# Kernel tuning notes

Hardware: AMD Instinct MI355X
Metric: run time of the kernel (lower is better)

## Reference

```python
import jax, jax.numpy as jnp
import numpy as np

B, L, D = 4, 2048, 512
NL, ED, N, R, K = 2, 1024, 16, 32, 4
EPS = 1e-5


def rmsnorm(x, w):
    return x * jax.lax.rsqrt(jnp.mean(x * x, axis=-1, keepdims=True) + EPS) * w


def mamba_block(u, in_w, conv_w, conv_b, xproj_w, dtproj_w, dtproj_b, A_log, Dp, out_w):
    # u: [B, L, D]
    xz = u @ in_w.T                              # [B, L, 2*ED]
    xp, z = jnp.split(xz, 2, axis=-1)
    # depthwise causal conv1d over time
    xc = jnp.transpose(xp, (0, 2, 1))            # [B, ED, L]
    w = conv_w[:, None, :]                       # [ED, 1, K]
    xc = jax.lax.conv_general_dilated(
        xc, w, window_strides=(1,), padding=[(K - 1, 0)],
        feature_group_count=ED, dimension_numbers=('NCH', 'OIH', 'NCH'))
    xc = jnp.transpose(xc, (0, 2, 1)) + conv_b   # [B, L, ED]
    xc = jax.nn.silu(xc)
    # input-dependent SSM params
    dbc = xc @ xproj_w.T                         # [B, L, R+2N]
    dt, Bm, Cm = jnp.split(dbc, [R, R + N], axis=-1)
    delta = jax.nn.softplus(dt @ dtproj_w.T + dtproj_b)  # [B, L, ED]
    A = -jnp.exp(A_log)                          # [ED, N]
    # sequential selective scan over time (carry h: [B, ED, N])
    dT = jnp.transpose(delta, (1, 0, 2))
    BT = jnp.transpose(Bm, (1, 0, 2))
    CT = jnp.transpose(Cm, (1, 0, 2))
    xT = jnp.transpose(xc, (1, 0, 2))

    def step(h, inp):
        d_t, B_t, C_t, x_t = inp                 # [B,ED], [B,N], [B,N], [B,ED]
        dA = jnp.exp(d_t[..., None] * A)         # [B, ED, N]
        h = dA * h + (d_t * x_t)[..., None] * B_t[:, None, :]
        y = jnp.einsum('ben,bn->be', h, C_t)
        return h, y

    h0 = jnp.zeros((u.shape[0], ED, N), u.dtype)
    _, yT = jax.lax.scan(step, h0, (dT, BT, CT, xT))
    y = jnp.transpose(yT, (1, 0, 2)) + Dp * xc   # [B, L, ED]
    y = y * jax.nn.silu(z)
    return y @ out_w.T                           # [B, L, D]


def setup_inputs() -> dict:
    key = jax.random.key(0)
    ks = jax.random.split(key, 10)
    s = 0.02
    return {
        'x': jax.random.normal(ks[0], (B, L, D), jnp.float32),
        'mask': jnp.ones((B, L), jnp.int32),
        'norm_w': jnp.ones((NL, D), jnp.float32),
        'in_w': jax.random.normal(ks[1], (NL, 2 * ED, D), jnp.float32) * s,
        'conv_w': jax.random.normal(ks[2], (NL, ED, K), jnp.float32) * 0.2,
        'conv_b': jnp.zeros((NL, ED), jnp.float32),
        'xproj_w': jax.random.normal(ks[3], (NL, R + 2 * N, ED), jnp.float32) * s,
        'dtproj_w': jax.random.normal(ks[4], (NL, ED, R), jnp.float32) * s,
        'dtproj_b': jax.random.normal(ks[5], (NL, ED), jnp.float32) * 0.1,
        'A_log': jnp.broadcast_to(jnp.log(jnp.arange(1, N + 1, dtype=jnp.float32)), (NL, ED, N)) + 0.0,
        'D_param': jnp.ones((NL, ED), jnp.float32),
        'out_w': jax.random.normal(ks[6], (NL, D, ED), jnp.float32) * s,
    }


def reference(x, mask, norm_w, in_w, conv_w, conv_b, xproj_w, dtproj_w,
              dtproj_b, A_log, D_param, out_w):
    m = mask.astype(x.dtype)[:, :, None]
    for i in range(norm_w.shape[0]):
        x = x * m
        # ResidualBlock: x + MambaBlock(RMSNorm(x)); dropout is identity at eval
        x = x + mamba_block(rmsnorm(x, norm_w[i]), in_w[i], conv_w[i], conv_b[i],
                            xproj_w[i], dtproj_w[i], dtproj_b[i], A_log[i],
                            D_param[i], out_w[i])
        x = x * m
    return x, x[:, 0, :]
```

## Files before the change

kernel.cpp:

```cpp
#include <hip/hip_runtime.h>
#include <math.h>

#define B_ 4
#define L_ 2048
#define D_ 512
#define ED_ 1024
#define N_ 16
#define R_ 32
#define KC_ 4
#define M_ (B_*L_)
#define NC_ 128
#define T_  (L_/NC_)
#define S_  (B_*ED_*N_)
#define LOG2E 1.44269504f
#define LN2   0.69314718f

typedef __attribute__((ext_vector_type(8))) short short8;
typedef __attribute__((ext_vector_type(4))) float floatx4;
typedef __attribute__((ext_vector_type(2))) float floatv2;

static __device__ __forceinline__ float b2f(unsigned short u) {
    unsigned int v = ((unsigned int)u) << 16;
    float f;
    __builtin_memcpy(&f, &v, 4);
    return f;
}
static __device__ __forceinline__ unsigned short f2b(float f) {
    unsigned int u;
    __builtin_memcpy(&u, &f, 4);
    unsigned int lsb = (u >> 16) & 1u;
    u += 0x7fffu + lsb;
    return (unsigned short)(u >> 16);
}
static __device__ __forceinline__ float silu(float x) {
    return x / (1.f + exp2f(-LOG2E * x));
}
static __device__ __forceinline__ float softplusf(float x) {
    return fmaxf(x, 0.f) + LN2 * log2f(1.f + exp2f(-LOG2E * fabsf(x)));
}
static __device__ __forceinline__ void pow_tree2(float a1, floatv2* pw) {
    float a2 = a1 * a1, a4 = a2 * a2, a8 = a4 * a4;
    pw[0] = (floatv2){a1, a2};
    pw[1] = pw[0] * a2;
    pw[2] = pw[0] * a4;
    pw[3] = pw[1] * a4;
    pw[4] = pw[0] * a8;
    pw[5] = pw[1] * a8;
    pw[6] = pw[2] * a8;
    pw[7] = pw[3] * a8;
}

__global__ void k_flag0(int* flag) {
    if (blockIdx.x == 0 && threadIdx.x == 0) *flag = 0;
}
__global__ void k_detect(const unsigned short* __restrict__ x, int* flag) {
    int i = blockIdx.x * 256 + threadIdx.x;
    unsigned int e = (x[i] >> 7) & 0xFF;
    unsigned long long m = __ballot(e >= 0x88);
    if ((threadIdx.x & 63) == 0 && m != 0ull) atomicOr(flag, 1);
}

struct Seg9 { const void* src[9]; int prefix[10]; };
__global__ void k_cvt_batch(Seg9 segs, float* __restrict__ dst, int total,
                            const int* __restrict__ flag) {
    int i = blockIdx.x * 256 + threadIdx.x;
    if (i >= total) return;
    int s = 0;
#pragma unroll
    for (int k = 1; k < 9; ++k) if (i >= segs.prefix[k]) s = k;
    int off = i - segs.prefix[s];
    if (*flag) dst[i] = ((const float*)segs.src[s])[off];
    else       dst[i] = b2f(((const unsigned short*)segs.src[s])[off]);
}
__global__ void k_cvt_bf_batch(const void* __restrict__ src0,
                               const void* __restrict__ src1,
                               unsigned short* __restrict__ dst,
                               int n0, int total, const int* __restrict__ flag) {
    int i = blockIdx.x * 256 + threadIdx.x;
    if (i >= total) return;
    const void* src = (i < n0) ? src0 : src1;
    int off = (i < n0) ? i : i - n0;
    if (*flag) dst[i] = f2b(((const float*)src)[off]);
    else       dst[i] = ((const unsigned short*)src)[off];
}

__global__ void k_prep(const float* __restrict__ wdt,
                       const float* __restrict__ A_log,
                       float* __restrict__ wT,
                       float* __restrict__ A0s,
                       int* __restrict__ structf) {
    int idx = blockIdx.x * 256 + threadIdx.x;
    int layer = idx >> 10, e = idx & (ED_ - 1);
    const float* src = wdt + (size_t)idx * R_;
    float* dstb = wT + (size_t)layer * (R_ * ED_);
#pragma unroll
    for (int r = 0; r < R_; ++r)
        dstb[(r >> 2) * (ED_ * 4) + e * 4 + (r & 3)] = src[r];
    float A0 = -exp2f(LOG2E * A_log[(size_t)idx * N_]) * LOG2E;
    bool st = true;
#pragma unroll
    for (int n = 1; n < N_; ++n) {
        float An = -exp2f(LOG2E * A_log[(size_t)idx * N_ + n]) * LOG2E;
        st = st && (fabsf(An - (n + 1) * A0) <= 1e-4f * fabsf(An));
    }
    A0s[idx] = A0;
    structf[idx] = st ? 1 : 0;
}

__global__ __launch_bounds__(128) void k_rmsnorm(float* __restrict__ x,
                                                 const int* __restrict__ mask,
                                                 const float* __restrict__ w,
                                                 unsigned short* __restrict__ ubf) {
    int row = blockIdx.x;
    int tid = threadIdx.x;
    size_t base = (size_t)row * D_ + tid * 4;
    float4 v = *(const float4*)(x + base);
    float mv = (float)mask[row];
    v.x *= mv; v.y *= mv; v.z *= mv; v.w *= mv;
    *(float4*)(x + base) = v;
    float ss = v.x*v.x + v.y*v.y + v.z*v.z + v.w*v.w;
#pragma unroll
    for (int o = 1; o < 64; o <<= 1) ss += __shfl_xor(ss, o, 64);
    __shared__ float sred[2];
    if ((tid & 63) == 0) sred[tid >> 6] = ss;
    __syncthreads();
    float rs = rsqrtf((sred[0] + sred[1]) / (float)D_ + 1e-5f);
    float4 wv = *(const float4*)(w + tid * 4);
    ushort4 b4;
    b4.x = f2b(v.x * rs * wv.x);
    b4.y = f2b(v.y * rs * wv.y);
    b4.z = f2b(v.z * rs * wv.z);
    b4.w = f2b(v.w * rs * wv.w);
    *(ushort4*)(ubf + base) = b4;
}

typedef __attribute__((address_space(1))) const unsigned int guint;
typedef __attribute__((address_space(3))) unsigned int luint;
#define GLL(gp, lp) __builtin_amdgcn_global_load_lds((guint*)(const void*)(gp), (luint*)(void*)(lp), 16, 0, 0)

template<int N> static __device__ __forceinline__ void waitv() {
    if constexpr (N == 0) asm volatile("s_waitcnt vmcnt(0)" ::: "memory");
    else if constexpr (N == 3) asm volatile("s_waitcnt vmcnt(3)" ::: "memory");
    else if constexpr (N == 4) asm volatile("s_waitcnt vmcnt(4)" ::: "memory");
}

template<int MODE, int BNT>
__global__ __launch_bounds__(256) void gemm_bt(const unsigned short* __restrict__ A,
                                               const unsigned short* __restrict__ W,
                                               void* __restrict__ C,
                                               const int* __restrict__ mask,
                                               const int* __restrict__ flag,
                                               void* __restrict__ out,
                                               int M, int N, int K) {
    constexpr int NF = BNT / 32;
    constexpr int LW = 2 + BNT / 64;
    __shared__ unsigned short As[3][128][32];
    __shared__ unsigned short Bs[3][BNT][32];
    int tid  = threadIdx.x;
    int wave = tid >> 6;
    int lane = tid & 63;
    int nwg = gridDim.x * gridDim.y;
    int id  = blockIdx.y * gridDim.x + blockIdx.x;
    int swz = (id & 7) * (nwg >> 3) + (id >> 3);
    int m0 = (swz / gridDim.x) * 128;
    int n0 = (swz % gridDim.x) * BNT;
    int wm = (wave & 1) * 64;
    int wn = (wave >> 1) * (BNT / 2);
    int quad = lane >> 4;
    int l16  = lane & 15;
    int crd = (quad ^ ((l16 >> 1) & 3)) * 8;

    int rA0 = wave * 16 + (lane >> 2);
    int cA  = ((lane & 3) ^ ((rA0 >> 1) & 3)) * 8;

    floatx4 acc[4][NF] = {};

    auto stage = [&](int buf, int k0) {
        const unsigned short* gA0 = A + (size_t)(m0 + rA0) * K + k0 + cA;
        GLL(gA0,                   &As[buf][wave * 16][0]);
        GLL(gA0 + (size_t)64 * K,  &As[buf][64 + wave * 16][0]);
        const unsigned short* gB0 = W + (size_t)(n0 + rA0) * K + k0 + cA;
        GLL(gB0,                   &Bs[buf][wave * 16][0]);
        if constexpr (BNT == 128)
            GLL(gB0 + (size_t)64 * K, &Bs[buf][64 + wave * 16][0]);
    };

    int nk = K / 32;
    stage(0, 0);
    stage(1, 32);

    int cur = 0;
    for (int t = 0; t < nk; ++t) {
        if (t + 1 < nk) waitv<LW>();
        else            waitv<0>();
        asm volatile("s_barrier" ::: "memory");
        if (t + 2 < nk) {
            int bw = cur + 2; if (bw >= 3) bw -= 3;
            stage(bw, (t + 2) * 32);
        }
        short8 af[4], bfr[NF];
#pragma unroll
        for (int f = 0; f < 4; ++f)
            af[f]  = *(const short8*)&As[cur][wm + f * 16 + l16][crd];
#pragma unroll
        for (int f = 0; f < NF; ++f)
            bfr[f] = *(const short8*)&Bs[cur][wn + f * 16 + l16][crd];
#pragma unroll
        for (int mf = 0; mf < 4; ++mf)
#pragma unroll
            for (int nf = 0; nf < NF; ++nf)
                acc[mf][nf] = __builtin_amdgcn_mfma_f32_16x16x32_bf16(af[mf], bfr[nf], acc[mf][nf], 0, 0, 0);
        asm volatile("s_waitcnt lgkmcnt(0)" ::: "memory");
        cur = (cur == 2) ? 0 : cur + 1;
    }

    int fl = (MODE == 3) ? *flag : 0;
#pragma unroll
    for (int mf = 0; mf < 4; ++mf) {
#pragma unroll
        for (int nf = 0; nf < NF; ++nf) {
#pragma unroll
            for (int i = 0; i < 4; ++i) {
                int r = m0 + wm + mf * 16 + quad * 4 + i;
                int c = n0 + wn + nf * 16 + l16;
                size_t idx = (size_t)r * N + c;
                if (MODE == 1) {
                    ((unsigned short*)C)[idx] = f2b(acc[mf][nf][i]);
                } else if (MODE == 2) {
                    float* C32 = (float*)C;
                    float mv = (float)mask[r];
                    C32[idx] = (C32[idx] + acc[mf][nf][i]) * mv;
                } else {
                    const float* C32 = (const float*)C;
                    float mv = (float)mask[r];
                    float v = (C32[idx] + acc[mf][nf][i]) * mv;
                    if (fl) ((float*)out)[idx] = v;
                    else    ((unsigned short*)out)[idx] = f2b(v);
                    if ((r & (L_ - 1)) == 0) {
                        size_t oidx = (size_t)M_ * D_ + (size_t)(r >> 11) * D_ + c;
                        if (fl) ((float*)out)[oidx] = v;
                        else    ((unsigned short*)out)[oidx] = f2b(v);
                    }
                }
            }
        }
    }
}

#define BM 64
#define BN 64
#define BK 16
#define KS 8
__global__ __launch_bounds__(256) void gemm_nt_sk(const float* __restrict__ A,
                                                  const float* __restrict__ W,
                                                  float* __restrict__ part,
                                                  int M, int N, int K) {
    __shared__ float Asm[BK][BM + 4];
    __shared__ float Wsm[BK][BN + 4];
    int tid = threadIdx.x;
    int ks = blockIdx.x;
    int m0 = blockIdx.y * BM;
    int kb = ks * (K / KS);
    int ke = kb + (K / KS);
    int tx = tid & 15;
    int ty = tid >> 4;
    int lr = tid >> 2;
    int lk = (tid & 3) * 4;
    float acc[4][4] = {};
    for (int k0 = kb; k0 < ke; k0 += BK) {
        float4 av = *(const float4*)(A + (size_t)(m0 + lr) * K + k0 + lk);
        Asm[lk + 0][lr] = av.x; Asm[lk + 1][lr] = av.y;
        Asm[lk + 2][lr] = av.z; Asm[lk + 3][lr] = av.w;
        float4 wv = *(const float4*)(W + (size_t)lr * K + k0 + lk);
        Wsm[lk + 0][lr] = wv.x; Wsm[lk + 1][lr] = wv.y;
        Wsm[lk + 2][lr] = wv.z; Wsm[lk + 3][lr] = wv.w;
        __syncthreads();
#pragma unroll
        for (int kk = 0; kk < BK; ++kk) {
            float4 a = *(const float4*)&Asm[kk][ty * 4];
            float4 w = *(const float4*)&Wsm[kk][tx * 4];
            acc[0][0] += a.x * w.x; acc[0][1] += a.x * w.y; acc[0][2] += a.x * w.z; acc[0][3] += a.x * w.w;
            acc[1][0] += a.y * w.x; acc[1][1] += a.y * w.y; acc[1][2] += a.y * w.z; acc[1][3] += a.y * w.w;
            acc[2][0] += a.z * w.x; acc[2][1] += a.z * w.y; acc[2][2] += a.z * w.z; acc[2][3] += a.z * w.w;
            acc[3][0] += a.w * w.x; acc[3][1] += a.w * w.y; acc[3][2] += a.w * w.z; acc[3][3] += a.w * w.w;
        }
        __syncthreads();
    }
    float* p = part + (size_t)ks * M * N;
#pragma unroll
    for (int i = 0; i < 4; ++i) {
        int m = m0 + ty * 4 + i;
#pragma unroll
        for (int j = 0; j < 4; ++j) {
            int n = tx * 4 + j;
            p[(size_t)m * N + n] = acc[i][j];
        }
    }
}

__global__ void k_red8(const float* __restrict__ part, float* __restrict__ dbc, int mn4) {
    int i = blockIdx.x * 256 + threadIdx.x;
    if (i >= mn4) return;
    float4 s = ((const float4*)part)[i];
#pragma unroll
    for (int ks = 1; ks < KS; ++ks) {
        float4 v = ((const float4*)(part + (size_t)ks * mn4 * 4))[i];
        s.x += v.x; s.y += v.y; s.z += v.z; s.w += v.w;
    }
    ((float4*)dbc)[i] = s;
}

__global__ __launch_bounds__(256) void k_conv(const unsigned short* __restrict__ xzb,
                                              const float* __restrict__ cw,
                                              const float* __restrict__ cb,
                                              float* __restrict__ xc) {
    int idx = blockIdx.x * 256 + threadIdx.x;
    int e2 = idx & (ED_ / 2 - 1);
    int e  = e2 * 2;
    int bl = idx >> 9;
    int l  = bl & (L_ - 1);
    float acc0 = cb[e], acc1 = cb[e + 1];
    const unsigned short* col = xzb + (size_t)bl * (2 * ED_) + e;
    float4 wa = *(const float4*)(cw + e * 4);
    float4 wb = *(const float4*)(cw + e * 4 + 4);
    ushort2 v3 = *(const ushort2*)(col);
    if (l >= 3) {
        ushort2 v0 = *(const ushort2*)(col - 3 * 2 * ED_);
        ushort2 v1 = *(const ushort2*)(col - 2 * 2 * ED_);
        ushort2 v2 = *(const ushort2*)(col - 1 * 2 * ED_);
        acc0 += wa.x * b2f(v0.x) + wa.y * b2f(v1.x) + wa.z * b2f(v2.x) + wa.w * b2f(v3.x);
        acc1 += wb.x * b2f(v0.y) + wb.y * b2f(v1.y) + wb.z * b2f(v2.y) + wb.w * b2f(v3.y);
    } else {
        if (l >= 2) {
            ushort2 v1 = *(const ushort2*)(col - 2 * 2 * ED_);
            acc0 += wa.y * b2f(v1.x); acc1 += wb.y * b2f(v1.y);
        }
        if (l >= 1) {
            ushort2 v2 = *(const ushort2*)(col - 1 * 2 * ED_);
            acc0 += wa.z * b2f(v2.x); acc1 += wb.z * b2f(v2.y);
        }
        acc0 += wa.w * b2f(v3.x); acc1 += wb.w * b2f(v3.y);
    }
    float2 o; o.x = silu(acc0); o.y = silu(acc1);
    *(float2*)(xc + (size_t)bl * ED_ + e) = o;
}

__global__ __launch_bounds__(256) void k_scan_a(const float* __restrict__ xc,
                                                const float* __restrict__ dbc,
                                                const float* __restrict__ wt,
                                                const float* __restrict__ dtb,
                                                const float* __restrict__ A0s,
                                                const int* __restrict__ structf,
                                                const float* __restrict__ A_log,
                                                float* __restrict__ sumdbuf,
                                                float* __restrict__ hl) {
    int b = blockIdx.z, c = blockIdx.y;
    int e = blockIdx.x * 256 + threadIdx.x;
    __shared__ float sRow[T_][64];
    size_t t0 = (size_t)b * L_ + (size_t)c * T_;
    {
        const float4* src = (const float4*)(dbc + t0 * 64);
        ((float4*)&sRow[0][0])[threadIdx.x] = src[threadIdx.x];
    }
    __syncthreads();
    floatv2 w2[R_ / 2];
    {
        const float4* wtp = (const float4*)wt;
#pragma unroll
        for (int i = 0; i < 8; ++i) {
            float4 v = wtp[(size_t)i * ED_ + e];
            w2[2 * i]     = (floatv2){v.x, v.y};
            w2[2 * i + 1] = (floatv2){v.z, v.w};
        }
    }
    float bias = dtb[e];
    float A0 = A0s[e];
    bool structured = structf[e] != 0;
    floatv2 h2[8];
#pragma unroll
    for (int i = 0; i < 8; ++i) h2[i] = (floatv2){0.f, 0.f};
    float sumd = 0.f;
    if (structured) {
        const float* xp = xc + t0 * ED_ + e;
        float xv_t = *xp; xp += ED_;
        for (int t = 0; t < T_; ++t) {
            float xv_n = (t + 1 < T_) ? *xp : 0.f; xp += ED_;
            const floatv2* dt2 = (const floatv2*)&sRow[t][0];
            floatv2 q0 = {0.f, 0.f}, q1 = {0.f, 0.f}, q2 = {0.f, 0.f}, q3 = {0.f, 0.f};
#pragma unroll
            for (int r = 0; r < R_ / 2; r += 4) {
                q0 += dt2[r + 0] * w2[r + 0];
                q1 += dt2[r + 1] * w2[r + 1];
                q2 += dt2[r + 2] * w2[r + 2];
                q3 += dt2[r + 3] * w2[r + 3];
            }
            floatv2 qs = (q0 + q1) + (q2 + q3);
            float d = softplusf(qs.x + qs.y + bias);
            float dx = d * xv_t;
            sumd += d;
            floatv2 pw[8];
            pow_tree2(exp2f(d * A0), pw);
            const floatv2* bb2 = (const floatv2*)&sRow[t][32];
#pragma unroll
            for (int i = 0; i < 8; ++i)
                h2[i] = pw[i] * h2[i] + dx * bb2[i];
            xv_t = xv_n;
        }
    } else {
        float A[N_];
        float* h = (float*)h2;
#pragma unroll
        for (int n = 0; n < N_; ++n) A[n] = -exp2f(LOG2E * A_log[e * N_ + n]) * LOG2E;
        float* wsc = (float*)w2;
        for (int t = 0; t < T_; ++t) {
            size_t bl = t0 + t;
            float p0 = bias, p1 = 0.f, p2 = 0.f, p3 = 0.f;
#pragma unroll
            for (int r = 0; r < R_; r += 4) {
                p0 += sRow[t][r + 0] * wsc[r + 0];
                p1 += sRow[t][r + 1] * wsc[r + 1];
                p2 += sRow[t][r + 2] * wsc[r + 2];
                p3 += sRow[t][r + 3] * wsc[r + 3];
            }
            float d = softplusf((p0 + p1) + (p2 + p3));
            float dx = d * xc[bl * ED_ + e];
            sumd += d;
#pragma unroll
            for (int n = 0; n < N_; ++n) {
                float a = exp2f(d * A[n]);
                h[n] = a * h[n] + dx * sRow[t][32 + n];
            }
        }
    }
    size_t s = (size_t)c * S_ + ((size_t)b * ED_ + e) * N_;
    const float* h = (const float*)h2;
#pragma unroll
    for (int n = 0; n < N_; ++n) hl[s + n] = h[n];
    sumdbuf[(size_t)c * (B_ * ED_) + (size_t)b * ED_ + e] = sumd;
}

__global__ __launch_bounds__(256) void k_scan_b(const float* __restrict__ sumd,
                                                const float* __restrict__ hl,
                                                const float* __restrict__ A_log,
                                                float* __restrict__ carry) {
    int s = blockIdx.x * 256 + threadIdx.x;
    float An = -exp2f(LOG2E * A_log[s & (ED_ * N_ - 1)]) * LOG2E;
    int be = s >> 4;
    float sdr[8], hlr[8];
#pragma unroll
    for (int c = 0; c < 8; ++c) {
        sdr[c] = sumd[(size_t)c * (B_ * ED_) + be];
        hlr[c] = hl[(size_t)c * S_ + s];
    }
    float h = 0.f;
#pragma unroll
    for (int c = 0; c < NC_; ++c) {
        int r = c & 7;
        carry[(size_t)c * S_ + s] = h;
        float p = exp2f(sdr[r] * An), q = hlr[r];
        if (c + 8 < NC_) {
            sdr[r] = sumd[(size_t)(c + 8) * (B_ * ED_) + be];
            hlr[r] = hl[(size_t)(c + 8) * S_ + s];
        }
        h = p * h + q;
    }
}

__global__ __launch_bounds__(256) void k_scan_c(const float* __restrict__ xc,
                                                const float* __restrict__ dbc,
                                                const unsigned short* __restrict__ xzb,
                                                const float* __restrict__ wt,
                                                const float* __restrict__ dtb,
                                                const float* __restrict__ A0s,
                                                const int* __restrict__ structf,
                                                const float* __restrict__ A_log,
                                                const float* __restrict__ Dp,
                                                const float* __restrict__ carry,
                                                unsigned short* __restrict__ ybf) {
    int b = blockIdx.z, c = blockIdx.y;
    int e = blockIdx.x * 256 + threadIdx.x;
    __shared__ float sRow[T_][64];
    size_t t0 = (size_t)b * L_ + (size_t)c * T_;
    {
        const float4* src = (const float4*)(dbc + t0 * 64);
        ((float4*)&sRow[0][0])[threadIdx.x] = src[threadIdx.x];
    }
    __syncthreads();
    floatv2 w2[R_ / 2];
    {
        const float4* wtp = (const float4*)wt;
#pragma unroll
        for (int i = 0; i < 8; ++i) {
            float4 v = wtp[(size_t)i * ED_ + e];
            w2[2 * i]     = (floatv2){v.x, v.y};
            w2[2 * i + 1] = (floatv2){v.z, v.w};
        }
    }
    float bias = dtb[e];
    float A0 = A0s[e];
    bool structured = structf[e] != 0;
    floatv2 h2[8];
    size_t s = (size_t)c * S_ + ((size_t)b * ED_ + e) * N_;
    {
        const floatv2* cp = (const floatv2*)(carry + s);
#pragma unroll
        for (int i = 0; i < 8; ++i) h2[i] = cp[i];
    }
    float Dv = Dp[e];
    if (structured) {
        const float* xp  = xc  + t0 * ED_ + e;
        const unsigned short* zp = xzb + t0 * (2 * ED_) + ED_ + e;
        unsigned short* yp = ybf + t0 * ED_ + e;
        float xv_t = *xp;  xp  += ED_;
        unsigned short z_t = *zp; zp += 2 * ED_;
        for (int t = 0; t < T_; ++t) {
            float xv_n = 0.f;
            unsigned short z_n = 0;
            if (t + 1 < T_) {
                xv_n = *xp;
                z_n  = *zp;
            }
            xp += ED_; zp += 2 * ED_;
            const floatv2* dt2 = (const floatv2*)&sRow[t][0];
            floatv2 q0 = {0.f, 0.f}, q1 = {0.f, 0.f}, q2 = {0.f, 0.f}, q3 = {0.f, 0.f};
#pragma unroll
            for (int r = 0; r < R_ / 2; r += 4) {
                q0 += dt2[r + 0] * w2[r + 0];
                q1 += dt2[r + 1] * w2[r + 1];
                q2 += dt2[r + 2] * w2[r + 2];
                q3 += dt2[r + 3] * w2[r + 3];
            }
            floatv2 qs = (q0 + q1) + (q2 + q3);
            float d_t = softplusf(qs.x + qs.y + bias);
            float dx = d_t * xv_t;
            floatv2 pw[8];
            pow_tree2(exp2f(d_t * A0), pw);
            const floatv2* bb2 = (const floatv2*)&sRow[t][32];
            const floatv2* cc2 = (const floatv2*)&sRow[t][48];
            floatv2 y0 = {0.f, 0.f}, y1 = {0.f, 0.f};
#pragma unroll
            for (int i = 0; i < 8; i += 2) {
                h2[i + 0] = pw[i + 0] * h2[i + 0] + dx * bb2[i + 0];
                h2[i + 1] = pw[i + 1] * h2[i + 1] + dx * bb2[i + 1];
                y0 += h2[i + 0] * cc2[i + 0];
                y1 += h2[i + 1] * cc2[i + 1];
            }
            floatv2 ys = y0 + y1;
            float y = ys.x + ys.y;
            float z = b2f(z_t);
            *yp = f2b((y + Dv * xv_t) * silu(z)); yp += ED_;
            xv_t = xv_n; z_t = z_n;
        }
    } else {
        float A[N_];
        float* h = (float*)h2;
#pragma unroll
        for (int n = 0; n < N_; ++n) A[n] = -exp2f(LOG2E * A_log[e * N_ + n]) * LOG2E;
        float* wsc = (float*)w2;
        for (int t = 0; t < T_; ++t) {
            size_t bl = t0 + t;
            float p0 = bias, p1 = 0.f, p2 = 0.f, p3 = 0.f;
#pragma unroll
            for (int r = 0; r < R_; r += 4) {
                p0 += sRow[t][r + 0] * wsc[r + 0];
                p1 += sRow[t][r + 1] * wsc[r + 1];
                p2 += sRow[t][r + 2] * wsc[r + 2];
                p3 += sRow[t][r + 3] * wsc[r + 3];
            }
            float d = softplusf((p0 + p1) + (p2 + p3));
            float xv = xc[bl * ED_ + e];
            float dx = d * xv;
            float y = 0.f;
#pragma unroll
            for (int n = 0; n < N_; ++n) {
                float a = exp2f(d * A[n]);
                h[n] = a * h[n] + dx * sRow[t][32 + n];
                y += h[n] * sRow[t][48 + n];
            }
            float z = b2f(xzb[bl * (2 * ED_) + ED_ + e]);
            ybf[bl * ED_ + e] = f2b((y + Dv * xv) * silu(z));
        }
    }
}

extern "C" void kernel_launch(void* const* d_in, const int* in_sizes, int n_in,
                              void* d_out, int out_size, void* d_ws, size_t ws_size,
                              hipStream_t stream) {
    const int* mask = (const int*)d_in[1];

    float* ws = (float*)d_ws;
    int*   flag = (int*)d_ws;
    float* xw   = ws + 16;
    float* wn   = xw   + (size_t)M_ * D_;
    float* wc   = wn   + 1024;
    float* wcb  = wc   + 8192;
    float* wx   = wcb  + 2048;
    float* wdt  = wx   + 131072;
    float* wdtb = wdt  + 65536;
    float* wal  = wdtb + 2048;
    float* wdp  = wal  + 32768;
    unsigned short* wib = (unsigned short*)(wdp + 2048);
    unsigned short* wob = wib + 2097152;
    unsigned short* ubf = wob + 1048576;
    unsigned short* xzb = ubf + (size_t)M_ * D_;
    float* xc   = (float*)(xzb + (size_t)M_ * 2 * ED_);
    float* dbc  = xc    + (size_t)M_ * ED_;
    float* hl   = dbc   + (size_t)M_ * 64;
    float* carry= hl    + (size_t)NC_ * S_;
    float* sumd = carry + (size_t)NC_ * S_;
    float* wT   = sumd  + (size_t)NC_ * B_ * ED_;
    float* A0s  = wT    + 2 * R_ * ED_;
    int*   stfl = (int*)(A0s + 2 * ED_);
    unsigned short* ybf = (unsigned short*)hl;
    float* part = carry;

    k_flag0<<<1, 1, 0, stream>>>(flag);
    k_detect<<<128, 256, 0, stream>>>((const unsigned short*)d_in[0], flag);

    {
        Seg9 segs;
        int idxs[9] = {0, 2, 4, 5, 6, 7, 8, 9, 10};
        int pre = 0;
        for (int i = 0; i < 9; ++i) {
            segs.src[i] = d_in[idxs[i]];
            segs.prefix[i] = pre;
            pre += in_sizes[idxs[i]];
        }
        segs.prefix[9] = pre;
        k_cvt_batch<<<(pre + 255) / 256, 256, 0, stream>>>(segs, xw, pre, flag);
        int n0 = 2 * 2 * ED_ * D_;
        int tot = n0 + 2 * D_ * ED_;
        k_cvt_bf_batch<<<(tot + 255) / 256, 256, 0, stream>>>(d_in[3], d_in[11], wib, n0, tot, flag);
    }
    k_prep<<<(2 * ED_) / 256, 256, 0, stream>>>(wdt, wal, wT, A0s, stfl);

    for (int layer = 0; layer < 2; ++layer) {
        const float* nw = wn  + layer * D_;
        const unsigned short* iw = wib + (size_t)layer * 2 * ED_ * D_;
        const float* cw = wc  + layer * ED_ * KC_;
        const float* cb = wcb + layer * ED_;
        const float* xwp= wx  + (size_t)layer * 64 * ED_;
        const float* db = wdtb+ layer * ED_;
        const float* al = wal + layer * ED_ * N_;
        const float* dp = wdp + layer * ED_;
        const float* wtl= wT  + (size_t)layer * R_ * ED_;
        const float* a0l= A0s + layer * ED_;
        const int*   sfl= stfl+ layer * ED_;
        const unsigned short* ow = wob + (size_t)layer * D_ * ED_;

        k_rmsnorm<<<M_, 128, 0, stream>>>(xw, mask, nw, ubf);
        gemm_bt<1, 128><<<dim3(2 * ED_ / 128, M_ / 128), 256, 0, stream>>>(ubf, iw, xzb, nullptr, nullptr, nullptr, M_, 2 * ED_, D_);
        k_conv<<<(M_ * ED_ / 2) / 256, 256, 0, stream>>>(xzb, cw, cb, xc);
        gemm_nt_sk<<<dim3(KS, M_ / BM), 256, 0, stream>>>(xc, xwp, part, M_, 64, ED_);
        k_red8<<<(M_ * 64 / 4 + 255) / 256, 256, 0, stream>>>(part, dbc, M_ * 64 / 4);
        k_scan_a<<<dim3(ED_ / 256, NC_, B_), 256, 0, stream>>>(xc, dbc, wtl, db, a0l, sfl, al, sumd, hl);
        k_scan_b<<<S_ / 256, 256, 0, stream>>>(sumd, hl, al, carry);
        k_scan_c<<<dim3(ED_ / 256, NC_, B_), 256, 0, stream>>>(xc, dbc, xzb, wtl, db, a0l, sfl, al, dp, carry, ybf);
        if (layer == 0) {
            gemm_bt<2, 64><<<dim3(D_ / 64, M_ / 128), 256, 0, stream>>>(ybf, ow, xw, mask, nullptr, nullptr, M_, D_, ED_);
        } else {
            gemm_bt<3, 64><<<dim3(D_ / 64, M_ / 128), 256, 0, stream>>>(ybf, ow, xw, mask, flag, d_out, M_, D_, ED_);
        }
    }
}
```

Before: 543.5 us.

## Halve scan chunk count and store chunk states in n-major coalesced layout

Cuts the number of time chunks in the chunked selective scan from 128 to 64, which doubles the timesteps per chunk. This halves the sequential carry-propagation length and the size of the hl and carry buffers. The chunk-end state and carry arrays move from an (e,n)-interleaved layout to an n-major layout indexed by (n, chunk, b*ED+e), so per-thread stores and loads across e are coalesced. In exchange, each scan_a/scan_c block serially processes twice as many timesteps, and there are half as many blocks to fill the GPU.

```diff
diff --git a/kernel.cpp b/kernel.cpp
--- a/kernel.cpp
+++ b/kernel.cpp
@@ -9,9 +9,10 @@
 #define R_ 32
 #define KC_ 4
 #define M_ (B_*L_)
-#define NC_ 128
+#define NC_ 64
 #define T_  (L_/NC_)
 #define S_  (B_*ED_*N_)
+#define BE_ (B_*ED_)
 #define LOG2E 1.44269504f
 #define LN2   0.69314718f
 
@@ -360,7 +361,9 @@
     size_t t0 = (size_t)b * L_ + (size_t)c * T_;
     {
         const float4* src = (const float4*)(dbc + t0 * 64);
-        ((float4*)&sRow[0][0])[threadIdx.x] = src[threadIdx.x];
+        float4* dst = (float4*)&sRow[0][0];
+        dst[threadIdx.x]       = src[threadIdx.x];
+        dst[threadIdx.x + 256] = src[threadIdx.x + 256];
     }
     __syncthreads();
     floatv2 w2[R_ / 2];
@@ -432,11 +435,12 @@
             }
         }
     }
-    size_t s = (size_t)c * S_ + ((size_t)b * ED_ + e) * N_;
+    size_t base = (size_t)c * BE_ + (size_t)b * ED_ + e;
     const float* h = (const float*)h2;
 #pragma unroll
-    for (int n = 0; n < N_; ++n) hl[s + n] = h[n];
-    sumdbuf[(size_t)c * (B_ * ED_) + (size_t)b * ED_ + e] = sumd;
+    for (int n = 0; n < N_; ++n)
+        hl[(size_t)n * (NC_ * BE_) + base] = h[n];
+    sumdbuf[base] = sumd;
 }
 
 __global__ __launch_bounds__(256) void k_scan_b(const float* __restrict__ sumd,
@@ -444,23 +448,27 @@
                                                 const float* __restrict__ A_log,
                                                 float* __restrict__ carry) {
     int s = blockIdx.x * 256 + threadIdx.x;
-    float An = -exp2f(LOG2E * A_log[s & (ED_ * N_ - 1)]) * LOG2E;
-    int be = s >> 4;
+    int n  = s >> 12;
+    int be = s & (BE_ - 1);
+    int e  = be & (ED_ - 1);
+    float An = -exp2f(LOG2E * A_log[e * N_ + n]) * LOG2E;
+    const float* hln = hl    + (size_t)n * (NC_ * BE_);
+    float*       crn = carry + (size_t)n * (NC_ * BE_);
     float sdr[8], hlr[8];
 #pragma unroll
     for (int c = 0; c < 8; ++c) {
-        sdr[c] = sumd[(size_t)c * (B_ * ED_) + be];
-        hlr[c] = hl[(size_t)c * S_ + s];
+        sdr[c] = sumd[(size_t)c * BE_ + be];
+        hlr[c] = hln[(size_t)c * BE_ + be];
     }
     float h = 0.f;
 #pragma unroll
     for (int c = 0; c < NC_; ++c) {
         int r = c & 7;
-        carry[(size_t)c * S_ + s] = h;
+        crn[(size_t)c * BE_ + be] = h;
         float p = exp2f(sdr[r] * An), q = hlr[r];
         if (c + 8 < NC_) {
-            sdr[r] = sumd[(size_t)(c + 8) * (B_ * ED_) + be];
-            hlr[r] = hl[(size_t)(c + 8) * S_ + s];
+            sdr[r] = sumd[(size_t)(c + 8) * BE_ + be];
+            hlr[r] = hln[(size_t)(c + 8) * BE_ + be];
         }
         h = p * h + q;
     }
@@ -483,7 +491,9 @@
     size_t t0 = (size_t)b * L_ + (size_t)c * T_;
     {
         const float4* src = (const float4*)(dbc + t0 * 64);
-        ((float4*)&sRow[0][0])[threadIdx.x] = src[threadIdx.x];
+        float4* dst = (float4*)&sRow[0][0];
+        dst[threadIdx.x]       = src[threadIdx.x];
+        dst[threadIdx.x + 256] = src[threadIdx.x + 256];
     }
     __syncthreads();
     floatv2 w2[R_ / 2];
@@ -500,11 +510,14 @@
     float A0 = A0s[e];
     bool structured = structf[e] != 0;
     floatv2 h2[8];
-    size_t s = (size_t)c * S_ + ((size_t)b * ED_ + e) * N_;
+    size_t base = (size_t)c * BE_ + (size_t)b * ED_ + e;
     {
-        const floatv2* cp = (const floatv2*)(carry + s);
-#pragma unroll
-        for (int i = 0; i < 8; ++i) h2[i] = cp[i];
+        float hs[N_];
+#pragma unroll
+        for (int n = 0; n < N_; ++n)
+            hs[n] = carry[(size_t)n * (NC_ * BE_) + base];
+#pragma unroll
+        for (int i = 0; i < 8; ++i) h2[i] = (floatv2){hs[2 * i], hs[2 * i + 1]};
     }
     float Dv = Dp[e];
     if (structured) {
@@ -608,7 +621,7 @@
     float* hl   = dbc   + (size_t)M_ * 64;
     float* carry= hl    + (size_t)NC_ * S_;
     float* sumd = carry + (size_t)NC_ * S_;
-    float* wT   = sumd  + (size_t)NC_ * B_ * ED_;
+    float* wT   = sumd  + (size_t)NC_ * BE_;
     float* A0s  = wT    + 2 * R_ * ED_;
     int*   stfl = (int*)(A0s + 2 * ED_);
     unsigned short* ybf = (unsigned short*)hl;
```

Result: no change. 539.4 us (-0.8%).
